# Kernel optimization log

Measured on AMD Instinct MI355X. Metric: run time of the kernel, lower is better.

The kernel has to match this reference:

```python
import jax, jax.numpy as jnp
import numpy as np


def setup_inputs() -> dict:
    key = jax.random.key(0)
    k1, k2, k3, k4 = jax.random.split(key, 4)
    pi = np.float32(np.pi)
    return {
        "bii": pi * jax.random.uniform(k1, (1,), dtype=jnp.float32),
        "bjj": pi * jax.random.uniform(k2, (1,), dtype=jnp.float32),
        "bij_real": pi * jax.random.uniform(k3, (1,), dtype=jnp.float32),
        "bij_img": pi * jax.random.uniform(k4, (1,), dtype=jnp.float32),
        "conn_i": 123,
        "conn_j": 4567,
        "N": 8192,
    }


def _block_exp(bii, bjj, bij_real, bij_img):
    """Closed-form exp(1j*H) for Hermitian 2x2 H = [[a, c],[conj(c), b]].

    exp(1j*H) = e^{1j*t} * (cos(r) I + 1j * sin(r)/r * (H - t I)),
    t = (a+b)/2, r = sqrt(((a-b)/2)^2 + |c|^2). Exact since B is zero
    outside the 2x2 block, matching torch.matrix_exp(1j*B).
    """
    a = bii[0]
    b = bjj[0]
    cr = bij_real[0]
    ci = bij_img[0]
    t = 0.5 * (a + b)
    d = 0.5 * (a - b)
    r = jnp.sqrt(d * d + cr * cr + ci * ci)
    safe_r = jnp.where(r > 0, r, jnp.ones_like(r))
    sinc = jnp.where(r > 0, jnp.sin(r) / safe_r, jnp.ones_like(r))
    cosr = jnp.cos(r)
    phase = jnp.exp(1j * t.astype(jnp.complex64))  # complex64 scalar
    c = (cr + 1j * ci).astype(jnp.complex64)
    e_ii = phase * (cosr + 1j * sinc * d)
    e_jj = phase * (cosr - 1j * sinc * d)
    e_ij = phase * (1j * sinc) * c
    e_ji = phase * (1j * sinc) * jnp.conj(c)
    return e_ii, e_jj, e_ij, e_ji


def reference(bii, bjj, bij_real, bij_img, conn_i, conn_j, N):
    e_ii, e_jj, e_ij, e_ji = _block_exp(bii, bjj, bij_real, bij_img)
    V = jnp.eye(N, dtype=jnp.complex64)
    rows = jnp.array([conn_i, conn_j, conn_i, conn_j])
    cols = jnp.array([conn_i, conn_j, conn_j, conn_i])
    vals = jnp.stack([e_ii, e_jj, e_ij, e_ji]).astype(jnp.complex64)
    V = V.at[rows, cols].set(vals)
    return V
```

## Files before the change

kernel.cpp:

```cpp
#include <hip/hip_runtime.h>
#include <math.h>

__global__ __launch_bounds__(256) void diag_patch_kernel(
    float* __restrict__ out, int out_size,
    const float* __restrict__ bii,
    const float* __restrict__ bjj,
    const float* __restrict__ bij_real,
    const float* __restrict__ bij_img,
    const int* __restrict__ conn_i,
    const int* __restrict__ conn_j,
    const int* __restrict__ Np)
{
    const int n = Np[0];
    const int stride = out_size / n;
    const int mult = stride / n;

    const int i = conn_i[0];
    const int j = conn_j[0];

    const int gid = blockIdx.x * blockDim.x + threadIdx.x;
    const int nth = gridDim.x * blockDim.x;

    for (int r = gid; r < n; r += nth) {
        if (r != i && r != j) {
            out[(size_t)r * stride + (size_t)mult * r] = 1.0f;
        }
    }

    if (gid != 0) return;

    const float a  = bii[0];
    const float b  = bjj[0];
    const float cr = bij_real[0];
    const float ci = bij_img[0];

    const float t = 0.5f * (a + b);
    const float d = 0.5f * (a - b);
    const float r = sqrtf(d * d + cr * cr + ci * ci);
    const float sinc = (r > 0.f) ? (sinf(r) / r) : 1.0f;
    const float cosr = cosf(r);
    const float pr = cosf(t);
    const float pi = sinf(t);

    const float sd = sinc * d;
    const float eii_r = pr * cosr - pi * sd;
    const float eii_i = pr * sd + pi * cosr;
    const float ejj_r = pr * cosr + pi * sd;
    const float ejj_i = -pr * sd + pi * cosr;
    const float sc_r = -sinc * ci;
    const float sc_i = sinc * cr;
    const float eij_r = pr * sc_r - pi * sc_i;
    const float eij_i = pr * sc_i + pi * sc_r;
    const float sj_r = sinc * ci;
    const float sj_i = sinc * cr;
    const float eji_r = pr * sj_r - pi * sj_i;
    const float eji_i = pr * sj_i + pi * sj_r;

    if (mult == 2) {
        size_t idx;
        idx = (size_t)i * stride + 2 * (size_t)i; out[idx] = eii_r; out[idx + 1] = eii_i;
        idx = (size_t)j * stride + 2 * (size_t)j; out[idx] = ejj_r; out[idx + 1] = ejj_i;
        idx = (size_t)i * stride + 2 * (size_t)j; out[idx] = eij_r; out[idx + 1] = eij_i;
        idx = (size_t)j * stride + 2 * (size_t)i; out[idx] = eji_r; out[idx + 1] = eji_i;
    } else {
        out[(size_t)i * stride + i] = eii_r;
        out[(size_t)j * stride + j] = ejj_r;
        out[(size_t)i * stride + j] = eij_r;
        out[(size_t)j * stride + i] = eji_r;
    }
}

extern "C" void kernel_launch(void* const* d_in, const int* in_sizes, int n_in,
                              void* d_out, int out_size, void* d_ws, size_t ws_size,
                              hipStream_t stream) {
    const float* bii      = (const float*)d_in[0];
    const float* bjj      = (const float*)d_in[1];
    const float* bij_real = (const float*)d_in[2];
    const float* bij_img  = (const float*)d_in[3];
    const int*   conn_i   = (const int*)d_in[4];
    const int*   conn_j   = (const int*)d_in[5];
    const int*   Np       = (const int*)d_in[6];

    float* out = (float*)d_out;

    hipMemsetAsync(d_out, 0, (size_t)out_size * sizeof(float), stream);

    diag_patch_kernel<<<dim3(64), dim3(256), 0, stream>>>(
        out, out_size, bii, bjj, bij_real, bij_img, conn_i, conn_j, Np);
}
```

Measured before the change: 261.9 us.

## Fuse memset and diagonal patch into one vectorized nontemporal fill kernel

```diff
diff --git a/kernel.cpp b/kernel.cpp
--- a/kernel.cpp
+++ b/kernel.cpp
@@ -1,8 +1,19 @@
 #include <hip/hip_runtime.h>
 #include <math.h>
 
-__global__ __launch_bounds__(256) void diag_patch_kernel(
-    float* __restrict__ out, int out_size,
+typedef float vfloat4 __attribute__((ext_vector_type(4)));
+
+__device__ __forceinline__ void set_lane(vfloat4& v, int k, float val) {
+    switch (k) {
+        case 0: v.x = val; break;
+        case 1: v.y = val; break;
+        case 2: v.z = val; break;
+        case 3: v.w = val; break;
+    }
+}
+
+__global__ __launch_bounds__(256) void fill_all_kernel(
+    vfloat4* __restrict__ out4, int out_size,
     const float* __restrict__ bii,
     const float* __restrict__ bjj,
     const float* __restrict__ bij_real,
@@ -14,59 +25,78 @@
     const int n = Np[0];
     const int stride = out_size / n;
     const int mult = stride / n;
-
+    const int ls = 31 - __clz(stride);
+    const int mask = stride - 1;
     const int i = conn_i[0];
     const int j = conn_j[0];
 
-    const int gid = blockIdx.x * blockDim.x + threadIdx.x;
-    const int nth = gridDim.x * blockDim.x;
+    const int n_f4 = out_size >> 2;
+    const int tid = blockIdx.x * 256 + threadIdx.x;
+    const int nth = gridDim.x * 256;
 
-    for (int r = gid; r < n; r += nth) {
-        if (r != i && r != j) {
-            out[(size_t)r * stride + (size_t)mult * r] = 1.0f;
+    #pragma unroll 4
+    for (int q = tid; q < n_f4; q += nth) {
+        const int f = q << 2;
+        const int row = f >> ls;
+        const int o = f & mask;
+
+        vfloat4 v = {0.f, 0.f, 0.f, 0.f};
+
+        const int k = row * mult - o;
+        if ((unsigned)k < 4u) set_lane(v, k, 1.0f);
+
+        if (row == i || row == j) {
+            const float a  = bii[0];
+            const float b  = bjj[0];
+            const float cr = bij_real[0];
+            const float ci = bij_img[0];
+
+            const float t  = 0.5f * (a + b);
+            const float dd = 0.5f * (a - b);
+            const float r  = sqrtf(dd * dd + cr * cr + ci * ci);
+            const float sinc = (r > 0.f) ? (sinf(r) / r) : 1.0f;
+            const float cosr = cosf(r);
+            const float pr = cosf(t);
+            const float pim = sinf(t);
+
+            const float sd = sinc * dd;
+            float eii_r = pr * cosr - pim * sd;
+            float eii_i = pr * sd + pim * cosr;
+            float ejj_r = pr * cosr + pim * sd;
+            float ejj_i = -pr * sd + pim * cosr;
+            const float scr = -sinc * ci;
+            const float sci =  sinc * cr;
+            float eij_r = pr * scr - pim * sci;
+            float eij_i = pr * sci + pim * scr;
+            const float sjr =  sinc * ci;
+            const float sji =  sinc * cr;
+            const float eji_r = pr * sjr - pim * sji;
+            const float eji_i = pr * sji + pim * sjr;
+
+            if (i == j) {
+                eii_r = eji_r; eii_i = eji_i;
+                ejj_r = eji_r; ejj_i = eji_i;
+                eij_r = eji_r; eij_i = eji_i;
+            }
+
+            float c0r, c0i, c1r, c1i;
+            if (row == i) { c0r = eii_r; c0i = eii_i; c1r = eij_r; c1i = eij_i; }
+            else          { c0r = eji_r; c0i = eji_i; c1r = ejj_r; c1i = ejj_i; }
+
+            if (mult == 2) {
+                const int k0 = 2 * i - o;
+                if ((unsigned)k0 < 4u) { set_lane(v, k0, c0r); set_lane(v, k0 + 1, c0i); }
+                const int k1 = 2 * j - o;
+                if ((unsigned)k1 < 4u) { set_lane(v, k1, c1r); set_lane(v, k1 + 1, c1i); }
+            } else {
+                const int k0 = i - o;
+                if ((unsigned)k0 < 4u) set_lane(v, k0, c0r);
+                const int k1 = j - o;
+                if ((unsigned)k1 < 4u) set_lane(v, k1, c1r);
+            }
         }
-    }
 
-    if (gid != 0) return;
-
-    const float a  = bii[0];
-    const float b  = bjj[0];
-    const float cr = bij_real[0];
-    const float ci = bij_img[0];
-
-    const float t = 0.5f * (a + b);
-    const float d = 0.5f * (a - b);
-    const float r = sqrtf(d * d + cr * cr + ci * ci);
-    const float sinc = (r > 0.f) ? (sinf(r) / r) : 1.0f;
-    const float cosr = cosf(r);
-    const float pr = cosf(t);
-    const float pi = sinf(t);
-
-    const float sd = sinc * d;
-    const float eii_r = pr * cosr - pi * sd;
-    const float eii_i = pr * sd + pi * cosr;
-    const float ejj_r = pr * cosr + pi * sd;
-    const float ejj_i = -pr * sd + pi * cosr;
-    const float sc_r = -sinc * ci;
-    const float sc_i = sinc * cr;
-    const float eij_r = pr * sc_r - pi * sc_i;
-    const float eij_i = pr * sc_i + pi * sc_r;
-    const float sj_r = sinc * ci;
-    const float sj_i = sinc * cr;
-    const float eji_r = pr * sj_r - pi * sj_i;
-    const float eji_i = pr * sj_i + pi * sj_r;
-
-    if (mult == 2) {
-        size_t idx;
-        idx = (size_t)i * stride + 2 * (size_t)i; out[idx] = eii_r; out[idx + 1] = eii_i;
-        idx = (size_t)j * stride + 2 * (size_t)j; out[idx] = ejj_r; out[idx + 1] = ejj_i;
-        idx = (size_t)i * stride + 2 * (size_t)j; out[idx] = eij_r; out[idx + 1] = eij_i;
-        idx = (size_t)j * stride + 2 * (size_t)i; out[idx] = eji_r; out[idx + 1] = eji_i;
-    } else {
-        out[(size_t)i * stride + i] = eii_r;
-        out[(size_t)j * stride + j] = ejj_r;
-        out[(size_t)i * stride + j] = eij_r;
-        out[(size_t)j * stride + i] = eji_r;
+        __builtin_nontemporal_store(v, out4 + q);
     }
 }
 
@@ -81,10 +111,11 @@
     const int*   conn_j   = (const int*)d_in[5];
     const int*   Np       = (const int*)d_in[6];
 
-    float* out = (float*)d_out;
+    const int n_f4 = out_size >> 2;
+    int blocks = (n_f4 + 255) / 256;
+    if (blocks > 2048) blocks = 2048;
 
-    hipMemsetAsync(d_out, 0, (size_t)out_size * sizeof(float), stream);
-
-    diag_patch_kernel<<<dim3(64), dim3(256), 0, stream>>>(
-        out, out_size, bii, bjj, bij_real, bij_img, conn_i, conn_j, Np);
+    fill_all_kernel<<<dim3(blocks), dim3(256), 0, stream>>>(
+        (vfloat4*)d_out, out_size, bii, bjj, bij_real, bij_img,
+        conn_i, conn_j, Np);
 }
```

Result: slower. 288.0 us (+10.0%).
